# Optimization experiments

Hardware: AMD Instinct MI355X
Metric: run time of the kernel (lower is better)

## Reference

```python
import jax, jax.numpy as jnp
import numpy as np

EPS = 1e-5
B, N, NODE_DIM, D, H, DK, FF, L = 16, 512, 2, 256, 8, 32, 512, 3


def _u(key, shape):
    s = 1.0 / np.sqrt(shape[-1])
    return jax.random.uniform(key, shape, minval=-s, maxval=s, dtype=jnp.float32)


def _bn(h, g, b):
    # BatchNorm1d in training mode over flattened (B*N, D): biased variance
    m = h.mean(axis=(0, 1))
    v = h.var(axis=(0, 1))
    return (h - m) / jnp.sqrt(v + EPS) * g + b


def _edge_bias(em, eW1, eb1, eW2, eb2, eW3, eb3):
    # MLP(1, [16,16,H]) applied to each scalar edge weight -> (H, B, N, N)
    e = em[..., None]                       # (B,N,N,1)
    t = jax.nn.relu(e @ eW1 + eb1)          # (B,N,N,16)
    t = jax.nn.relu(t @ eW2 + eb2)          # (B,N,N,16)
    t = t @ eW3 + eb3                       # (B,N,N,H)
    return jnp.transpose(t, (3, 0, 1, 2))   # (H,B,N,N)


def _mha(h, Wq, Wk, Wv, Wo, bias):
    dk = Wq.shape[-1]
    Q = jnp.einsum('bnd,hdk->hbnk', h, Wq)
    K = jnp.einsum('bnd,hdk->hbnk', h, Wk)
    V = jnp.einsum('bnd,hdk->hbnk', h, Wv)
    scores = jnp.einsum('hbqk,hbnk->hbqn', Q, K) * (1.0 / jnp.sqrt(jnp.asarray(dk, h.dtype)))
    if bias is not None:
        scores = scores + bias
    attn = jax.nn.softmax(scores, axis=-1)
    heads = jnp.einsum('hbqn,hbnk->hbqk', attn, V)
    return jnp.einsum('hbqk,hke->bqe', heads, Wo)


def setup_inputs() -> dict:
    key = jax.random.key(0)
    ks = jax.random.split(key, 24)
    inp = {
        'x': jax.random.normal(ks[0], (B, N, NODE_DIM), dtype=jnp.float32),
        'edge_matrix': jax.random.uniform(ks[1], (B, N, N), dtype=jnp.float32),
        'init_W': _u(ks[2], (NODE_DIM, D)),
        'init_b': _u(ks[3], (D,)),
        'Wq': _u(ks[4], (L, H, D, DK)),
        'Wk': _u(ks[5], (L, H, D, DK)),
        'Wv': _u(ks[6], (L, H, D, DK)),
        'Wo': _u(ks[7], (L, H, DK, D)),
        'eW1': _u(ks[8], (1, 16)),
        'eb1': _u(ks[9], (16,)),
        'eW2': _u(ks[10], (16, 16)),
        'eb2': _u(ks[11], (16,)),
        'eW3': _u(ks[12], (16, H)),
        'eb3': _u(ks[13], (H,)),
        'bn1_g': jnp.ones((L, D), jnp.float32),
        'bn1_b': jnp.zeros((L, D), jnp.float32),
        'ffW1': _u(ks[14], (L, D, FF)),
        'ffb1': _u(ks[15], (L, FF)),
        'ffW2': _u(ks[16], (L, FF, D)),
        'ffb2': _u(ks[17], (L, D)),
        'bn2_g': jnp.ones((L, D), jnp.float32),
        'bn2_b': jnp.zeros((L, D), jnp.float32),
    }
    return inp


def reference(x, edge_matrix, init_W, init_b, Wq, Wk, Wv, Wo,
              eW1, eb1, eW2, eb2, eW3, eb3,
              bn1_g, bn1_b, ffW1, ffb1, ffW2, ffb2, bn2_g, bn2_b):
    h = x @ init_W + init_b                          # init_embed: (B,N,D)
    bias0 = _edge_bias(edge_matrix, eW1, eb1, eW2, eb2, eW3, eb3)
    for l in range(L):
        b_l = bias0 if l < 1 else None               # n_edge_encode_layers = 1
        h = h + _mha(h, Wq[l], Wk[l], Wv[l], Wo[l], b_l)
        h = _bn(h, bn1_g[l], bn1_b[l])
        h = h + (jax.nn.relu(h @ ffW1[l] + ffb1[l]) @ ffW2[l] + ffb2[l])
        h = _bn(h, bn2_g[l], bn2_b[l])
    graph_embed = h.mean(axis=1)                     # add_graph_dim == 0
    return (h, graph_embed)
```

## Files before the change

### kernel.cpp

```cpp
#include <hip/hip_runtime.h>

#define BB    16
#define NNN   512
#define DDIM  256
#define HH    8
#define DKK   32
#define FFF   512
#define MROWS 8192
#define LUTN  4096

using u16    = unsigned short;
using bf16x8 = __attribute__((ext_vector_type(8))) short;
using f32x4  = __attribute__((ext_vector_type(4))) float;

__device__ __forceinline__ float bf2f(u16 u) { return __uint_as_float(((unsigned)u) << 16); }
__device__ __forceinline__ u16 f2bf(float f) {
    unsigned u = __float_as_uint(f);
    return (u16)((u + 0x7fffu + ((u >> 16) & 1u)) >> 16);
}

__global__ __launch_bounds__(256) void init_embed_kernel(
    const float* __restrict__ x, const float* __restrict__ W,
    const float* __restrict__ b, float* __restrict__ h,
    u16* __restrict__ hhi, u16* __restrict__ hlo)
{
    size_t row = blockIdx.x;
    int c = threadIdx.x;
    float x0 = x[row * 2 + 0], x1 = x[row * 2 + 1];
    float v = x0 * W[c] + x1 * W[DDIM + c] + b[c];
    size_t o = row * DDIM + c;
    h[o] = v;
    u16 hv = f2bf(v);
    hhi[o] = hv;
    hlo[o] = f2bf(v - bf2f(hv));
}

#define WT_LSTR 1048576
__global__ __launch_bounds__(256) void wsplit_kernel(
    const float* __restrict__ Wq, const float* __restrict__ Wk,
    const float* __restrict__ Wv, const float* __restrict__ Wo,
    const float* __restrict__ ffW1, const float* __restrict__ ffW2,
    u16* __restrict__ Wt)
{
    int fid = blockIdx.x * 256 + threadIdx.x;
    int l = fid >> 19, r = fid & 524287;
    u16* base = Wt + (size_t)l * WT_LSTR;
    float v; int off_hi, off_lo;
    if (r < 196608) {
        int n = r >> 8, k = r & 255;
        int mat = n >> 8, hd = (n & 255) >> 5, dk = n & 31;
        const float* Wsel = (mat == 0) ? Wq : ((mat == 1) ? Wk : Wv);
        v = Wsel[(((size_t)l * HH + hd) * DDIM + k) * DKK + dk];
        off_hi = r; off_lo = r + 196608;
    } else if (r < 262144) {
        int r2 = r - 196608;
        int n = r2 >> 8, k = r2 & 255;
        int hd = k >> 5, dk = k & 31;
        v = Wo[(((size_t)l * HH + hd) * DKK + dk) * DDIM + n];
        off_hi = 393216 + r2; off_lo = 458752 + r2;
    } else if (r < 393216) {
        int r3 = r - 262144;
        int n = r3 >> 8, k = r3 & 255;
        v = ffW1[((size_t)l * DDIM + k) * FFF + n];
        off_hi = 524288 + r3; off_lo = 655360 + r3;
    } else {
        int r4 = r - 393216;
        int n = r4 >> 9, k = r4 & 511;
        v = ffW2[((size_t)l * FFF + k) * DDIM + n];
        off_hi = 786432 + r4; off_lo = 917504 + r4;
    }
    u16 hv = f2bf(v);
    base[off_hi] = hv;
    base[off_lo] = f2bf(v - bf2f(hv));
}

__global__ __launch_bounds__(256) void build_lut_kernel(
    const float* __restrict__ eW1, const float* __restrict__ eb1,
    const float* __restrict__ eW2, const float* __restrict__ eb2,
    const float* __restrict__ eW3, const float* __restrict__ eb3,
    float* __restrict__ lut)
{
    int i = blockIdx.x * 256 + threadIdx.x;
    if (i > LUTN) return;
    float e = (float)i * (1.0f / LUTN);
    float t1[16], t2[16];
    #pragma unroll
    for (int a = 0; a < 16; ++a) t1[a] = fmaxf(e * eW1[a] + eb1[a], 0.0f);
    #pragma unroll
    for (int j = 0; j < 16; ++j) {
        float s = eb2[j];
        #pragma unroll
        for (int a = 0; a < 16; ++a) s += t1[a] * eW2[a * 16 + j];
        t2[j] = fmaxf(s, 0.0f);
    }
    #pragma unroll
    for (int hd = 0; hd < 8; ++hd) {
        float s = eb3[hd];
        #pragma unroll
        for (int j = 0; j < 16; ++j) s += t2[j] * eW3[j * 8 + hd];
        lut[(size_t)i * 8 + hd] = s;
    }
}

__global__ __launch_bounds__(256) void edge_bias_kernel(
    const float* __restrict__ edge, const float* __restrict__ lut,
    u16* __restrict__ bout)
{
    size_t idx = (size_t)blockIdx.x * 256 + threadIdx.x;
    float e = edge[idx];
    float f = e * (float)LUTN;
    f = fminf(fmaxf(f, 0.0f), (float)LUTN - 0.0001f);
    int i0 = (int)f;
    float fr = f - (float)i0;
    const float4* r = (const float4*)(lut + (size_t)i0 * 8);
    float4 a0 = r[0], a1 = r[1], b0 = r[2], b1 = r[3];
    float o[8];
    o[0] = a0.x + fr * (b0.x - a0.x);
    o[1] = a0.y + fr * (b0.y - a0.y);
    o[2] = a0.z + fr * (b0.z - a0.z);
    o[3] = a0.w + fr * (b0.w - a0.w);
    o[4] = a1.x + fr * (b1.x - a1.x);
    o[5] = a1.y + fr * (b1.y - a1.y);
    o[6] = a1.z + fr * (b1.z - a1.z);
    o[7] = a1.w + fr * (b1.w - a1.w);
    #pragma unroll
    for (int hd = 0; hd < 8; ++hd)
        bout[(size_t)hd * (size_t)BB * NNN * NNN + idx] = f2bf(o[hd]);
}

__global__ __launch_bounds__(256, 2) void gemm2_kernel(
    const u16* __restrict__ Ah_g, const u16* __restrict__ Al_g, int K,
    const u16* __restrict__ Bth, const u16* __restrict__ Btl, int N,
    float* __restrict__ Cf,
    u16* __restrict__ Chi, u16* __restrict__ Clo,
    const float* __restrict__ bias, int relu,
    const float* __restrict__ res)
{
    __shared__ __align__(16) u16 Ah[128][72];
    __shared__ __align__(16) u16 Al[128][72];
    int m0 = blockIdx.y * 128, n0 = blockIdx.x * 64;
    int tid = threadIdx.x, lid = tid & 63, wid = tid >> 6;
    int wm = wid >> 1, wn = wid & 1;
    int l15 = lid & 15, l4 = lid >> 4;

    f32x4 acc[4][2] = {};

    for (int k0 = 0; k0 < K; k0 += 64) {
        #pragma unroll
        for (int j = 0; j < 4; ++j) {
            int c = tid + 256 * j;
            int row = c >> 3, col8 = c & 7;
            bf16x8 vh = *(const bf16x8*)&Ah_g[(size_t)(m0 + row) * K + k0 + col8 * 8];
            bf16x8 vl = *(const bf16x8*)&Al_g[(size_t)(m0 + row) * K + k0 + col8 * 8];
            *(bf16x8*)&Ah[row][col8 * 8] = vh;
            *(bf16x8*)&Al[row][col8 * 8] = vl;
        }
        __syncthreads();
        #pragma unroll
        for (int ks = 0; ks < 2; ++ks) {
            int ko = ks * 32;
            bf16x8 afh[4], afl[4], bfh[2], bfl[2];
            #pragma unroll
            for (int mi = 0; mi < 4; ++mi) {
                afh[mi] = *(const bf16x8*)&Ah[wm * 64 + mi * 16 + l15][ko + l4 * 8];
                afl[mi] = *(const bf16x8*)&Al[wm * 64 + mi * 16 + l15][ko + l4 * 8];
            }
            #pragma unroll
            for (int ni = 0; ni < 2; ++ni) {
                size_t brow = (size_t)(n0 + wn * 32 + ni * 16 + l15) * K + k0 + ko + l4 * 8;
                bfh[ni] = *(const bf16x8*)&Bth[brow];
                bfl[ni] = *(const bf16x8*)&Btl[brow];
            }
            #pragma unroll
            for (int mi = 0; mi < 4; ++mi)
                #pragma unroll
                for (int ni = 0; ni < 2; ++ni) {
                    acc[mi][ni] = __builtin_amdgcn_mfma_f32_16x16x32_bf16(
                        afh[mi], bfh[ni], acc[mi][ni], 0, 0, 0);
                    acc[mi][ni] = __builtin_amdgcn_mfma_f32_16x16x32_bf16(
                        afh[mi], bfl[ni], acc[mi][ni], 0, 0, 0);
                    acc[mi][ni] = __builtin_amdgcn_mfma_f32_16x16x32_bf16(
                        afl[mi], bfh[ni], acc[mi][ni], 0, 0, 0);
                }
        }
        __syncthreads();
    }
    #pragma unroll
    for (int mi = 0; mi < 4; ++mi) {
        #pragma unroll
        for (int ni = 0; ni < 2; ++ni) {
            #pragma unroll
            for (int r = 0; r < 4; ++r) {
                int row = m0 + wm * 64 + mi * 16 + l4 * 4 + r;
                int col = n0 + wn * 32 + ni * 16 + l15;
                float v = acc[mi][ni][r];
                if (bias) v += bias[col];
                if (relu) v = fmaxf(v, 0.0f);
                if (res)  v += res[(size_t)row * N + col];
                size_t o = (size_t)row * N + col;
                if (Cf) Cf[o] = v;
                if (Chi) {
                    u16 hv = f2bf(v);
                    Chi[o] = hv;
                    Clo[o] = f2bf(v - bf2f(hv));
                }
            }
        }
    }
}

__global__ __launch_bounds__(256, 2) void attn_flash_kernel(
    const u16* __restrict__ qkv_hi, const u16* __restrict__ qkv_lo,
    const u16* __restrict__ bias,
    u16* __restrict__ attb_hi, u16* __restrict__ attb_lo)
{
    __shared__ __align__(16) u16 Kh[128][40];
    __shared__ __align__(16) u16 Kl[128][40];
    __shared__ __align__(16) u16 Vt[32][136];
    __shared__ __align__(16) u16 Pw[4][16][136];
    int wg = blockIdx.x;
    int logical = (wg & 7) * 64 + (wg >> 3);
    int qc = logical & 3, hd = (logical >> 2) & 7, b = logical >> 5;
    int tid = threadIdx.x, lid = tid & 63, w = tid >> 6;
    int l15 = lid & 15, l4 = lid >> 4;

    const u16* baseh = qkv_hi + (size_t)b * 512 * 768;
    const u16* basel = qkv_lo + (size_t)b * 512 * 768;

    int q0 = qc * 128 + w * 32;
    bf16x8 qh[2], ql[2];
    #pragma unroll
    for (int qf = 0; qf < 2; ++qf) {
        size_t qrow = (size_t)(q0 + qf * 16 + l15) * 768 + hd * 32 + l4 * 8;
        qh[qf] = *(const bf16x8*)&baseh[qrow];
        ql[qf] = *(const bf16x8*)&basel[qrow];
    }

    f32x4 oacc[2][2] = {};
    float mrow[2][4], lrow[2][4];
    #pragma unroll
    for (int qf = 0; qf < 2; ++qf)
        #pragma unroll
        for (int r = 0; r < 4; ++r) { mrow[qf][r] = -1e30f; lrow[qf][r] = 0.0f; }

    const float scale = 0.17677669529663687f;

    for (int kt = 0; kt < 4; ++kt) {
        __syncthreads();
        #pragma unroll
        for (int it = 0; it < 4; ++it) {
            int idx = tid + 256 * it;
            int n = idx >> 3, c4 = idx & 7;
            size_t grow = (size_t)(kt * 128 + n) * 768 + 256 + hd * 32 + c4 * 4;
            ushort4 kh4 = *(const ushort4*)&baseh[grow];
            ushort4 kl4 = *(const ushort4*)&basel[grow];
            ushort4 vh4 = *(const ushort4*)&baseh[grow + 256];
            *(ushort4*)&Kh[n][c4 * 4] = kh4;
            *(ushort4*)&Kl[n][c4 * 4] = kl4;
            Vt[c4 * 4 + 0][n] = vh4.x;
            Vt[c4 * 4 + 1][n] = vh4.y;
            Vt[c4 * 4 + 2][n] = vh4.z;
            Vt[c4 * 4 + 3][n] = vh4.w;
        }
        __syncthreads();

        f32x4 sacc[2][8];
        #pragma unroll
        for (int ct = 0; ct < 8; ++ct) {
            bf16x8 bh = *(const bf16x8*)&Kh[ct * 16 + l15][l4 * 8];
            bf16x8 bl = *(const bf16x8*)&Kl[ct * 16 + l15][l4 * 8];
            #pragma unroll
            for (int qf = 0; qf < 2; ++qf) {
                f32x4 z = {0.0f, 0.0f, 0.0f, 0.0f};
                z = __builtin_amdgcn_mfma_f32_16x16x32_bf16(qh[qf], bh, z, 0, 0, 0);
                z = __builtin_amdgcn_mfma_f32_16x16x32_bf16(ql[qf], bh, z, 0, 0, 0);
                sacc[qf][ct] = __builtin_amdgcn_mfma_f32_16x16x32_bf16(qh[qf], bl, z, 0, 0, 0);
            }
        }

        if (bias) {
            #pragma unroll
            for (int qf = 0; qf < 2; ++qf) {
                size_t brow0 = (((size_t)hd * BB + b) * NNN + q0 + qf * 16 + l4 * 4) * NNN
                               + kt * 128 + l15;
                #pragma unroll
                for (int ct = 0; ct < 8; ++ct)
                    #pragma unroll
                    for (int r = 0; r < 4; ++r)
                        sacc[qf][ct][r] = sacc[qf][ct][r] * scale +
                            bf2f(bias[brow0 + (size_t)r * NNN + ct * 16]);
            }
        } else {
            #pragma unroll
            for (int qf = 0; qf < 2; ++qf)
                #pragma unroll
                for (int ct = 0; ct < 8; ++ct)
                    #pragma unroll
                    for (int r = 0; r < 4; ++r)
                        sacc[qf][ct][r] *= scale;
        }

        #pragma unroll
        for (int qf = 0; qf < 2; ++qf) {
            #pragma unroll
            for (int r = 0; r < 4; ++r) {
                float pm = sacc[qf][0][r];
                #pragma unroll
                for (int ct = 1; ct < 8; ++ct) pm = fmaxf(pm, sacc[qf][ct][r]);
                #pragma unroll
                for (int msk = 1; msk < 16; msk <<= 1) pm = fmaxf(pm, __shfl_xor(pm, msk));
                float mnew = fmaxf(mrow[qf][r], pm);
                float corr = __expf(mrow[qf][r] - mnew);
                mrow[qf][r] = mnew;
                float ls = 0.0f;
                #pragma unroll
                for (int ct = 0; ct < 8; ++ct) {
                    float p = __expf(sacc[qf][ct][r] - mnew);
                    sacc[qf][ct][r] = p;
                    ls += p;
                }
                #pragma unroll
                for (int msk = 1; msk < 16; msk <<= 1) ls += __shfl_xor(ls, msk);
                lrow[qf][r] = lrow[qf][r] * corr + ls;
                oacc[qf][0][r] *= corr;
                oacc[qf][1][r] *= corr;
            }
        }

        #pragma unroll
        for (int qf = 0; qf < 2; ++qf) {
            #pragma unroll
            for (int ct = 0; ct < 8; ++ct)
                #pragma unroll
                for (int r = 0; r < 4; ++r)
                    Pw[w][l4 * 4 + r][ct * 16 + l15] = f2bf(sacc[qf][ct][r]);
            #pragma unroll
            for (int ks = 0; ks < 4; ++ks) {
                bf16x8 pa = *(const bf16x8*)&Pw[w][l15][ks * 32 + l4 * 8];
                #pragma unroll
                for (int dc = 0; dc < 2; ++dc) {
                    bf16x8 vb = *(const bf16x8*)&Vt[dc * 16 + l15][ks * 32 + l4 * 8];
                    oacc[qf][dc] = __builtin_amdgcn_mfma_f32_16x16x32_bf16(
                        pa, vb, oacc[qf][dc], 0, 0, 0);
                }
            }
        }
    }

    #pragma unroll
    for (int qf = 0; qf < 2; ++qf)
        #pragma unroll
        for (int dc = 0; dc < 2; ++dc)
            #pragma unroll
            for (int r = 0; r < 4; ++r) {
                float o = oacc[qf][dc][r] / lrow[qf][r];
                size_t oi = ((size_t)b * NNN + q0 + qf * 16 + l4 * 4 + r) * DDIM
                            + hd * 32 + dc * 16 + l15;
                u16 hv = f2bf(o);
                attb_hi[oi] = hv;
                attb_lo[oi] = f2bf(o - bf2f(hv));
            }
}

__global__ void zero_stats_kernel(float* stats)
{
    stats[threadIdx.x] = 0.0f;
    stats[256 + threadIdx.x] = 0.0f;
}

__global__ __launch_bounds__(256) void bn_stats_kernel(
    const float* __restrict__ X, float* __restrict__ stats)
{
    int c = threadIdx.x;
    size_t r0 = (size_t)blockIdx.x * 32;
    float s = 0.0f, ss = 0.0f;
    for (int r = 0; r < 32; ++r) {
        float v = X[(r0 + r) * DDIM + c];
        s += v; ss += v * v;
    }
    atomicAdd(&stats[c], s);
    atomicAdd(&stats[256 + c], ss);
}

__global__ __launch_bounds__(256) void bn_apply_kernel(
    const float* __restrict__ X, float* __restrict__ Y,
    u16* __restrict__ Yhi, u16* __restrict__ Ylo,
    const float* __restrict__ stats,
    const float* __restrict__ g, const float* __restrict__ bb)
{
    int c = threadIdx.x;
    float mean = stats[c] * (1.0f / MROWS);
    float var  = stats[256 + c] * (1.0f / MROWS) - mean * mean;
    float inv  = rsqrtf(var + 1e-5f);
    float gg = g[c] * inv;
    float off = bb[c] - mean * gg;
    size_t r0 = (size_t)blockIdx.x * 8;
    #pragma unroll
    for (int r = 0; r < 8; ++r) {
        size_t o = (r0 + r) * DDIM + c;
        float y = X[o] * gg + off;
        Y[o] = y;
        if (Yhi) {
            u16 hv = f2bf(y);
            Yhi[o] = hv;
            Ylo[o] = f2bf(y - bf2f(hv));
        }
    }
}

__global__ __launch_bounds__(256) void graph_embed_kernel(
    const float* __restrict__ outh, float* __restrict__ outg)
{
    int c = threadIdx.x, b = blockIdx.x;
    float s = 0.0f;
    for (int n = 0; n < NNN; ++n)
        s += outh[((size_t)b * NNN + n) * DDIM + c];
    outg[b * DDIM + c] = s * (1.0f / NNN);
}

extern "C" void kernel_launch(void* const* d_in, const int* in_sizes, int n_in,
                              void* d_out, int out_size, void* d_ws, size_t ws_size,
                              hipStream_t stream)
{
    const float* x     = (const float*)d_in[0];
    const float* edge  = (const float*)d_in[1];
    const float* initW = (const float*)d_in[2];
    const float* initb = (const float*)d_in[3];
    const float* Wq    = (const float*)d_in[4];
    const float* Wk    = (const float*)d_in[5];
    const float* Wv    = (const float*)d_in[6];
    const float* Wo    = (const float*)d_in[7];
    const float* eW1   = (const float*)d_in[8];
    const float* eb1   = (const float*)d_in[9];
    const float* eW2   = (const float*)d_in[10];
    const float* eb2   = (const float*)d_in[11];
    const float* eW3   = (const float*)d_in[12];
    const float* eb3   = (const float*)d_in[13];
    const float* bn1g  = (const float*)d_in[14];
    const float* bn1b  = (const float*)d_in[15];
    const float* ffW1  = (const float*)d_in[16];
    const float* ffb1  = (const float*)d_in[17];
    const float* ffW2  = (const float*)d_in[18];
    const float* ffb2  = (const float*)d_in[19];
    const float* bn2g  = (const float*)d_in[20];
    const float* bn2b  = (const float*)d_in[21];

    char* ws = (char*)d_ws;
    float* h      = (float*)(ws);
    float* h2     = (float*)(ws + ((size_t)8  << 20));
    u16*   h_hi   = (u16*)  (ws + ((size_t)16 << 20));
    u16*   h_lo   = (u16*)  (ws + ((size_t)20 << 20));
    u16*   qkv_hi = (u16*)  (ws + ((size_t)24 << 20));
    u16*   qkv_lo = (u16*)  (ws + ((size_t)36 << 20));
    float* stats  = (float*)(ws + ((size_t)48 << 20));
    float* lut    = (float*)(ws + ((size_t)48 << 20) + 4096);
    u16*   Wt     = (u16*)  (ws + ((size_t)49 << 20));
    u16*   bias   = (u16*)  (ws + ((size_t)56 << 20));
    u16*   attb_hi = h_hi;
    u16*   attb_lo = h_lo;
    u16*   ff_hi   = qkv_hi;
    u16*   ff_lo   = qkv_lo;
    float* outh  = (float*)d_out;
    float* outg  = outh + (size_t)MROWS * DDIM;

    wsplit_kernel<<<6144, 256, 0, stream>>>(Wq, Wk, Wv, Wo, ffW1, ffW2, Wt);
    init_embed_kernel<<<MROWS, 256, 0, stream>>>(x, initW, initb, h, h_hi, h_lo);
    build_lut_kernel<<<17, 256, 0, stream>>>(eW1, eb1, eW2, eb2, eW3, eb3, lut);
    edge_bias_kernel<<<(BB * NNN * NNN) / 256, 256, 0, stream>>>(edge, lut, bias);

    for (int l = 0; l < 3; ++l) {
        u16* WL = Wt + (size_t)l * WT_LSTR;
        gemm2_kernel<<<dim3(12, 64), 256, 0, stream>>>(
            h_hi, h_lo, 256, WL, WL + 196608, 768,
            nullptr, qkv_hi, qkv_lo, nullptr, 0, nullptr);
        attn_flash_kernel<<<512, 256, 0, stream>>>(
            qkv_hi, qkv_lo, (l == 0) ? bias : (const u16*)nullptr, attb_hi, attb_lo);
        gemm2_kernel<<<dim3(4, 64), 256, 0, stream>>>(
            attb_hi, attb_lo, 256, WL + 393216, WL + 458752, 256,
            h2, nullptr, nullptr, nullptr, 0, h);
        zero_stats_kernel<<<1, 256, 0, stream>>>(stats);
        bn_stats_kernel<<<256, 256, 0, stream>>>(h2, stats);
        bn_apply_kernel<<<1024, 256, 0, stream>>>(
            h2, h, h_hi, h_lo, stats, bn1g + l * 256, bn1b + l * 256);
        gemm2_kernel<<<dim3(8, 64), 256, 0, stream>>>(
            h_hi, h_lo, 256, WL + 524288, WL + 655360, 512,
            nullptr, ff_hi, ff_lo, ffb1 + l * 512, 1, nullptr);
        gemm2_kernel<<<dim3(4, 64), 256, 0, stream>>>(
            ff_hi, ff_lo, 512, WL + 786432, WL + 917504, 256,
            h2, nullptr, nullptr, ffb2 + l * 256, 0, h);
        zero_stats_kernel<<<1, 256, 0, stream>>>(stats);
        bn_stats_kernel<<<256, 256, 0, stream>>>(h2, stats);
        if (l == 2)
            bn_apply_kernel<<<1024, 256, 0, stream>>>(
                h2, outh, nullptr, nullptr, stats, bn2g + l * 256, bn2b + l * 256);
        else
            bn_apply_kernel<<<1024, 256, 0, stream>>>(
                h2, h, h_hi, h_lo, stats, bn2g + l * 256, bn2b + l * 256);
    }
    graph_embed_kernel<<<BB, 256, 0, stream>>>(outh, outg);
}
```

Baseline: 680.8 us.

## Fuse BatchNorm statistics into GEMM epilogue and preallocate per-layer stats buffers

Per-column sum and sum-of-squares for BatchNorm are now accumulated in the epilogue of the output-projection and FF2 GEMMs, reduced through shared memory and added atomically. This removes the separate bn_stats pass over h2 and its zeroing launch. All six per-layer stats buffers are zeroed once up front, and the LUT builder now stages its small MLP weights in shared memory. The cost is extra epilogue work, two more block barriers and float atomics whose ordering is non-deterministic.

```diff
diff --git a/kernel.cpp b/kernel.cpp
--- a/kernel.cpp
+++ b/kernel.cpp
@@ -80,24 +80,31 @@
     const float* __restrict__ eW3, const float* __restrict__ eb3,
     float* __restrict__ lut)
 {
-    int i = blockIdx.x * 256 + threadIdx.x;
+    __shared__ float sm[440];
+    int t = threadIdx.x;
+    if (t < 16) { sm[t] = eW1[t]; sm[16 + t] = eb1[t]; sm[288 + t] = eb2[t]; }
+    if (t < 256) sm[32 + t] = eW2[t];
+    if (t < 128) sm[304 + t] = eW3[t];
+    if (t < 8)   sm[432 + t] = eb3[t];
+    __syncthreads();
+    int i = blockIdx.x * 256 + t;
     if (i > LUTN) return;
     float e = (float)i * (1.0f / LUTN);
     float t1[16], t2[16];
     #pragma unroll
-    for (int a = 0; a < 16; ++a) t1[a] = fmaxf(e * eW1[a] + eb1[a], 0.0f);
+    for (int a = 0; a < 16; ++a) t1[a] = fmaxf(e * sm[a] + sm[16 + a], 0.0f);
     #pragma unroll
     for (int j = 0; j < 16; ++j) {
-        float s = eb2[j];
-        #pragma unroll
-        for (int a = 0; a < 16; ++a) s += t1[a] * eW2[a * 16 + j];
+        float s = sm[288 + j];
+        #pragma unroll
+        for (int a = 0; a < 16; ++a) s += t1[a] * sm[32 + a * 16 + j];
         t2[j] = fmaxf(s, 0.0f);
     }
     #pragma unroll
     for (int hd = 0; hd < 8; ++hd) {
-        float s = eb3[hd];
-        #pragma unroll
-        for (int j = 0; j < 16; ++j) s += t2[j] * eW3[j * 8 + hd];
+        float s = sm[432 + hd];
+        #pragma unroll
+        for (int j = 0; j < 16; ++j) s += t2[j] * sm[304 + j * 8 + hd];
         lut[(size_t)i * 8 + hd] = s;
     }
 }
@@ -134,7 +141,8 @@
     float* __restrict__ Cf,
     u16* __restrict__ Chi, u16* __restrict__ Clo,
     const float* __restrict__ bias, int relu,
-    const float* __restrict__ res)
+    const float* __restrict__ res,
+    float* __restrict__ bnstats)
 {
     __shared__ __align__(16) u16 Ah[128][72];
     __shared__ __align__(16) u16 Al[128][72];
@@ -185,6 +193,7 @@
         }
         __syncthreads();
     }
+    float psum[2] = {0.0f, 0.0f}, psq[2] = {0.0f, 0.0f};
     #pragma unroll
     for (int mi = 0; mi < 4; ++mi) {
         #pragma unroll
@@ -204,7 +213,30 @@
                     Chi[o] = hv;
                     Clo[o] = f2bf(v - bf2f(hv));
                 }
-            }
+                if (bnstats) { psum[ni] += v; psq[ni] += v * v; }
+            }
+        }
+    }
+    if (bnstats) {
+        float* red = (float*)&Ah[0][0];
+        int base = ((((wm * 2 + wn) * 4 + l4) * 16 + l15) * 4);
+        __syncthreads();
+        #pragma unroll
+        for (int ni = 0; ni < 2; ++ni) {
+            red[base + ni * 2 + 0] = psum[ni];
+            red[base + ni * 2 + 1] = psq[ni];
+        }
+        __syncthreads();
+        if (tid < 128) {
+            int col = tid & 63, which = tid >> 6;
+            int wn_ = col >> 5, ni_ = (col >> 4) & 1, l15_ = col & 15;
+            float s = 0.0f;
+            #pragma unroll
+            for (int wm_ = 0; wm_ < 2; ++wm_)
+                #pragma unroll
+                for (int l4_ = 0; l4_ < 4; ++l4_)
+                    s += red[((((wm_ * 2 + wn_) * 4 + l4_) * 16 + l15_) * 4) + ni_ * 2 + which];
+            atomicAdd(&bnstats[which * 256 + n0 + col], s);
         }
     }
 }
@@ -364,22 +396,8 @@
 
 __global__ void zero_stats_kernel(float* stats)
 {
-    stats[threadIdx.x] = 0.0f;
-    stats[256 + threadIdx.x] = 0.0f;
-}
-
-__global__ __launch_bounds__(256) void bn_stats_kernel(
-    const float* __restrict__ X, float* __restrict__ stats)
-{
-    int c = threadIdx.x;
-    size_t r0 = (size_t)blockIdx.x * 32;
-    float s = 0.0f, ss = 0.0f;
-    for (int r = 0; r < 32; ++r) {
-        float v = X[(r0 + r) * DDIM + c];
-        s += v; ss += v * v;
-    }
-    atomicAdd(&stats[c], s);
-    atomicAdd(&stats[256 + c], ss);
+    int i = blockIdx.x * 256 + threadIdx.x;
+    if (i < 3072) stats[i] = 0.0f;
 }
 
 __global__ __launch_bounds__(256) void bn_apply_kernel(
@@ -452,8 +470,8 @@
     u16*   h_lo   = (u16*)  (ws + ((size_t)20 << 20));
     u16*   qkv_hi = (u16*)  (ws + ((size_t)24 << 20));
     u16*   qkv_lo = (u16*)  (ws + ((size_t)36 << 20));
-    float* stats  = (float*)(ws + ((size_t)48 << 20));
-    float* lut    = (float*)(ws + ((size_t)48 << 20) + 4096);
+    float* statsA = (float*)(ws + ((size_t)48 << 20));
+    float* lut    = (float*)(ws + ((size_t)48 << 20) + 16384);
     u16*   Wt     = (u16*)  (ws + ((size_t)49 << 20));
     u16*   bias   = (u16*)  (ws + ((size_t)56 << 20));
     u16*   attb_hi = h_hi;
@@ -467,35 +485,34 @@
     init_embed_kernel<<<MROWS, 256, 0, stream>>>(x, initW, initb, h, h_hi, h_lo);
     build_lut_kernel<<<17, 256, 0, stream>>>(eW1, eb1, eW2, eb2, eW3, eb3, lut);
     edge_bias_kernel<<<(BB * NNN * NNN) / 256, 256, 0, stream>>>(edge, lut, bias);
+    zero_stats_kernel<<<12, 256, 0, stream>>>(statsA);
 
     for (int l = 0; l < 3; ++l) {
         u16* WL = Wt + (size_t)l * WT_LSTR;
+        float* st1 = statsA + (size_t)(l * 2 + 0) * 512;
+        float* st2 = statsA + (size_t)(l * 2 + 1) * 512;
         gemm2_kernel<<<dim3(12, 64), 256, 0, stream>>>(
             h_hi, h_lo, 256, WL, WL + 196608, 768,
-            nullptr, qkv_hi, qkv_lo, nullptr, 0, nullptr);
+            nullptr, qkv_hi, qkv_lo, nullptr, 0, nullptr, nullptr);
         attn_flash_kernel<<<512, 256, 0, stream>>>(
             qkv_hi, qkv_lo, (l == 0) ? bias : (const u16*)nullptr, attb_hi, attb_lo);
         gemm2_kernel<<<dim3(4, 64), 256, 0, stream>>>(
             attb_hi, attb_lo, 256, WL + 393216, WL + 458752, 256,
-            h2, nullptr, nullptr, nullptr, 0, h);
-        zero_stats_kernel<<<1, 256, 0, stream>>>(stats);
-        bn_stats_kernel<<<256, 256, 0, stream>>>(h2, stats);
+            h2, nullptr, nullptr, nullptr, 0, h, st1);
         bn_apply_kernel<<<1024, 256, 0, stream>>>(
-            h2, h, h_hi, h_lo, stats, bn1g + l * 256, bn1b + l * 256);
+            h2, h, h_hi, h_lo, st1, bn1g + l * 256, bn1b + l * 256);
         gemm2_kernel<<<dim3(8, 64), 256, 0, stream>>>(
             h_hi, h_lo, 256, WL + 524288, WL + 655360, 512,
-            nullptr, ff_hi, ff_lo, ffb1 + l * 512, 1, nullptr);
+            nullptr, ff_hi, ff_lo, ffb1 + l * 512, 1, nullptr, nullptr);
         gemm2_kernel<<<dim3(4, 64), 256, 0, stream>>>(
             ff_hi, ff_lo, 512, WL + 786432, WL + 917504, 256,
-            h2, nullptr, nullptr, ffb2 + l * 256, 0, h);
-        zero_stats_kernel<<<1, 256, 0, stream>>>(stats);
-        bn_stats_kernel<<<256, 256, 0, stream>>>(h2, stats);
+            h2, nullptr, nullptr, ffb2 + l * 256, 0, h, st2);
         if (l == 2)
             bn_apply_kernel<<<1024, 256, 0, stream>>>(
-                h2, outh, nullptr, nullptr, stats, bn2g + l * 256, bn2b + l * 256);
+                h2, outh, nullptr, nullptr, st2, bn2g + l * 256, bn2b + l * 256);
         else
             bn_apply_kernel<<<1024, 256, 0, stream>>>(
-                h2, h, h_hi, h_lo, stats, bn2g + l * 256, bn2b + l * 256);
+                h2, h, h_hi, h_lo, st2, bn2g + l * 256, bn2b + l * 256);
     }
     graph_embed_kernel<<<BB, 256, 0, stream>>>(outh, outg);
 }
```

New measurement: 624.4 us. 1.09x faster.
